# Performance work log

Measured on AMD Instinct MI355X. Metric: run time of the kernel, lower is better.

## Reference

```python
import jax, jax.numpy as jnp
import numpy as np
import math

N_HEADS = 16
D_HEAD = 64
D_MODEL = 1024
ROPE_THETA = 10000.0


def setup_inputs() -> dict:
    key = jax.random.key(0)
    k1, k2, k3 = jax.random.split(key, 3)
    B, T = 2, 2048
    x = jax.random.normal(k1, (B, T, D_MODEL), dtype=jnp.float32)
    # torch Linear(in, out) weight has shape (out, in); store transposed (in, out)
    # so forward is x @ w. Scale like default init to keep activations sane.
    w_qkv = jax.random.normal(k2, (D_MODEL, 3 * D_MODEL), dtype=jnp.float32) / math.sqrt(D_MODEL)
    w_o = jax.random.normal(k3, (D_MODEL, D_MODEL), dtype=jnp.float32) / math.sqrt(D_MODEL)
    return {"x": x, "w_qkv": w_qkv, "w_o": w_o}


def _build_rope(T, dtype):
    inv_freq = 1.0 / (ROPE_THETA ** (jnp.arange(0, D_HEAD, 2, dtype=jnp.float32) / D_HEAD))
    t = jnp.arange(T, dtype=jnp.float32)
    freqs = jnp.outer(t, inv_freq)            # [T, D_HEAD/2]
    emb = jnp.concatenate([freqs, freqs], -1)  # [T, D_HEAD]
    return jnp.cos(emb).astype(dtype), jnp.sin(emb).astype(dtype)


def _apply_rope(x, cos, sin):
    # x: [B, T, H, D_HEAD]; cos/sin broadcast as [1, T, 1, D_HEAD]
    x1, x2 = jnp.split(x, 2, axis=-1)
    rotated = jnp.concatenate([-x2, x1], axis=-1)
    return x * cos + rotated * sin


def reference(x, w_qkv, w_o):
    B, T, D = x.shape
    qkv = (x @ w_qkv).reshape(B, T, 3, N_HEADS, D_HEAD)
    q, k, v = qkv[:, :, 0], qkv[:, :, 1], qkv[:, :, 2]  # [B, T, H, Dh]
    cos, sin = _build_rope(T, x.dtype)
    cos = cos[None, :, None, :]
    sin = sin[None, :, None, :]
    q = _apply_rope(q, cos, sin)
    k = _apply_rope(k, cos, sin)
    scale = 1.0 / math.sqrt(D_HEAD)
    # full [B, H, T, T] scores (faithful to the manual matmul-softmax-matmul)
    attn = jnp.einsum("bthd,bshd->bhts", q, k) * scale
    attn = jax.nn.softmax(attn, axis=-1)
    out = jnp.einsum("bhts,bshd->bthd", attn, v).reshape(B, T, D)
    return out @ w_o
```

## Files before the change

kernel.cpp:

```cpp
#include <hip/hip_runtime.h>
#include <cstdint>

typedef unsigned short ushort_t;
typedef __attribute__((ext_vector_type(8))) short v8s;
typedef __attribute__((ext_vector_type(4))) short v4s;
typedef __attribute__((ext_vector_type(2))) unsigned v2u;
typedef __attribute__((ext_vector_type(4))) float v4f;

#define MFMA(a, b, c) __builtin_amdgcn_mfma_f32_16x16x32_bf16(a, b, c, 0, 0, 0)
#define QSCALE 0.18033688011112042f

__device__ __forceinline__ float bf2f(ushort_t u) {
    union { unsigned u; float f; } x; x.u = ((unsigned)u) << 16; return x.f;
}
__device__ __forceinline__ short f2bf(float f) {
    union { float f; unsigned u; } x; x.f = f;
    unsigned r = x.u + 0x7fffu + ((x.u >> 16) & 1u);
    return (short)(r >> 16);
}

__global__ void detect_dtype(const unsigned* __restrict__ x, int* __restrict__ flag) {
    __shared__ int cnt;
    if (threadIdx.x == 0) cnt = 0;
    __syncthreads();
    unsigned w = x[threadIdx.x];
    int e = (w >> 7) & 0xFF;
    int hit = ((e >= 96 && e <= 135) || (w & 0xFFFFu) == 0) ? 1 : 0;
    atomicAdd(&cnt, hit);
    __syncthreads();
    if (threadIdx.x == 0) *flag = (cnt >= 160) ? 1 : 0;
}

__global__ __launch_bounds__(256) void cvt_x(const void* __restrict__ xin,
                                             ushort_t* __restrict__ xb,
                                             const int* __restrict__ flagp, int n8) {
    int i = blockIdx.x * 256 + threadIdx.x;
    if (i >= n8) return;
    if (*flagp) {
        ((v8s*)xb)[i] = ((const v8s*)xin)[i];
    } else {
        const float* xf = (const float*)xin + (size_t)i * 8;
        v8s o;
        #pragma unroll
        for (int j = 0; j < 8; ++j) o[j] = f2bf(xf[j]);
        ((v8s*)xb)[i] = o;
    }
}

__global__ __launch_bounds__(256) void cvt_transpose(const void* __restrict__ in,
                                                     ushort_t* __restrict__ out,
                                                     const int* __restrict__ flagp,
                                                     int R, int C) {
    __shared__ ushort_t tile[32][33];
    int bx = blockIdx.x * 32, by = blockIdx.y * 32;
    int tx = threadIdx.x, ty = threadIdx.y;
    int isbf = *flagp;
    for (int i = ty; i < 32; i += 8) {
        size_t idx = (size_t)(by + i) * C + bx + tx;
        tile[i][tx] = isbf ? ((const ushort_t*)in)[idx]
                           : (ushort_t)f2bf(((const float*)in)[idx]);
    }
    __syncthreads();
    for (int i = ty; i < 32; i += 8) out[(size_t)(bx + i) * R + by + tx] = tile[tx][i];
}

__global__ __launch_bounds__(256) void rope_table(float* __restrict__ tab) {
    int idx = blockIdx.x * 256 + threadIdx.x;
    int t = idx >> 5, d = idx & 31;
    float inv_freq = __expf(-(float)d * 0.28782313662425575f);
    float ang = (float)t * inv_freq;
    float sn, cs;
    sincosf(ang, &sn, &cs);
    tab[t * 64 + d]      = bf2f((ushort_t)f2bf(cs));
    tab[t * 64 + 32 + d] = bf2f((ushort_t)f2bf(sn));
}

template <int MODE>
__global__ __launch_bounds__(256) void gemm_bt(const ushort_t* __restrict__ A,
                                               const ushort_t* __restrict__ BT,
                                               void* __restrict__ C,
                                               const int* __restrict__ flagp,
                                               int M, int N, int K,
                                               ushort_t* __restrict__ Qp,
                                               ushort_t* __restrict__ Kp,
                                               ushort_t* __restrict__ Vp,
                                               const float* __restrict__ tab) {
    __shared__ __align__(16) ushort_t As[128 * 32];
    __shared__ __align__(16) ushort_t Bs[128 * 32];
    int tid = threadIdx.x;
    int lane = tid & 63;
    int lr = lane & 15, lc = lane >> 4;
    int w = tid >> 6;
    int wr = (w >> 1) * 64, wc = (w & 1) * 64;
    int m0 = blockIdx.y * 128, n0 = blockIdx.x * 128;

    int c0 = tid, c1 = tid + 256;
    int r0 = c0 >> 2, s0 = c0 & 3;
    int r1 = c1 >> 2, s1 = c1 & 3;

    v4f acc[4][4] = {};

    for (int kt = 0; kt < K; kt += 32) {
        v8s a0 = *(const v8s*)(A + (size_t)(m0 + r0) * K + kt + s0 * 8);
        v8s a1 = *(const v8s*)(A + (size_t)(m0 + r1) * K + kt + s1 * 8);
        v8s b0 = *(const v8s*)(BT + (size_t)(n0 + r0) * K + kt + s0 * 8);
        v8s b1 = *(const v8s*)(BT + (size_t)(n0 + r1) * K + kt + s1 * 8);
        __syncthreads();
        *(v8s*)(As + (size_t)c0 * 8) = a0;
        *(v8s*)(As + (size_t)c1 * 8) = a1;
        *(v8s*)(Bs + (size_t)c0 * 8) = b0;
        *(v8s*)(Bs + (size_t)c1 * 8) = b1;
        __syncthreads();

        v8s af[4], bfr[4];
        #pragma unroll
        for (int i = 0; i < 4; ++i)
            af[i] = *(const v8s*)(As + (wr + i * 16 + lr) * 32 + lc * 8);
        #pragma unroll
        for (int j = 0; j < 4; ++j)
            bfr[j] = *(const v8s*)(Bs + (wc + j * 16 + lr) * 32 + lc * 8);
        #pragma unroll
        for (int i = 0; i < 4; ++i)
            #pragma unroll
            for (int j = 0; j < 4; ++j)
                acc[i][j] = MFMA(af[i], bfr[j], acc[i][j]);
    }

    if (MODE == 1) {
        int store_f32 = (*flagp == 0);
        #pragma unroll
        for (int i = 0; i < 4; ++i)
            #pragma unroll
            for (int j = 0; j < 4; ++j)
                #pragma unroll
                for (int r = 0; r < 4; ++r) {
                    int row = m0 + wr + i * 16 + lc * 4 + r;
                    int col = n0 + wc + j * 16 + lr;
                    if (store_f32)
                        ((float*)C)[(size_t)row * N + col] = acc[i][j][r];
                    else
                        ((ushort_t*)C)[(size_t)row * N + col] = (ushort_t)f2bf(acc[i][j][r]);
                }
    } else {
        int region = n0 >> 10;
        int h = ((n0 & 1023) + wc) >> 6;
        if (region < 2) {
            const float sc = (region == 0) ? QSCALE : 1.0f;
            ushort_t* dst = (region == 0) ? Qp : Kp;
            #pragma unroll
            for (int i = 0; i < 4; ++i)
                #pragma unroll
                for (int j = 0; j < 2; ++j) {
                    int d = j * 16 + lr;
                    #pragma unroll
                    for (int r = 0; r < 4; ++r) {
                        int tg = m0 + wr + i * 16 + lc * 4 + r;
                        int b = tg >> 11, tt = tg & 2047;
                        float cs = tab[tt * 64 + d], sn = tab[tt * 64 + 32 + d];
                        float x1 = acc[i][j][r], x2 = acc[i][j + 2][r];
                        size_t base = ((size_t)(b * 16 + h) * 2048 + tt) * 64 + d;
                        dst[base]      = (ushort_t)f2bf((x1 * cs - x2 * sn) * sc);
                        dst[base + 32] = (ushort_t)f2bf((x2 * cs + x1 * sn) * sc);
                    }
                }
        } else {
            #pragma unroll
            for (int i = 0; i < 4; ++i)
                #pragma unroll
                for (int j = 0; j < 4; ++j) {
                    int d = j * 16 + lr;
                    int tg0 = m0 + wr + i * 16 + lc * 4;
                    int b = tg0 >> 11, tt = tg0 & 2047;
                    v4s pk;
                    #pragma unroll
                    for (int r = 0; r < 4; ++r) pk[r] = f2bf(acc[i][j][r]);
                    size_t base = (size_t)(b * 16 + h) * 131072 + (size_t)(tt >> 5) * 2048
                                + (size_t)d * 32 + (tt & 31);
                    *(v4s*)(Vp + base) = pk;
                }
        }
    }
}

__global__ __launch_bounds__(256) void attn(const ushort_t* __restrict__ Qr,
                                            const ushort_t* __restrict__ Kr,
                                            const ushort_t* __restrict__ Vt,
                                            ushort_t* __restrict__ AO) {
    __shared__ __align__(16) char lds[53248];
    int tid = threadIdx.x, lane = tid & 63, W = tid >> 6;
    int lr = lane & 15, lc = lane >> 4;
    int qsub = W & 1, sh = W >> 1;
    int L = blockIdx.x;
    int bh = (L & 7) * 4 + ((L >> 3) & 3);
    int qt = L >> 5;
    int q0 = qt * 128 + qsub * 64;
    int b = bh >> 4, h = bh & 15;
    const ushort_t* Qb = Qr + ((size_t)bh * 2048 + q0) * 64;
    const ushort_t* Kb = Kr + (size_t)bh * 131072 + (size_t)sh * 65536;
    const ushort_t* Vb = Vt + (size_t)bh * 131072 + (size_t)sh * 65536;
    ushort_t* Pw  = (ushort_t*)(lds + 32768 + W * 5120);
    ushort_t* KsG = (ushort_t*)(lds + sh * 16384);
    ushort_t* VsG = (ushort_t*)(lds + sh * 16384 + 8192);

    int gt = tid & 127;
    int c0 = gt, c1 = gt + 128;
    int kr0 = c0 >> 3, kc0 = c0 & 7, kr1 = c1 >> 3, kc1 = c1 & 7;
    const ushort_t* Kg0 = Kb + (size_t)kr0 * 64 + kc0 * 8;
    const ushort_t* Kg1 = Kb + (size_t)kr1 * 64 + kc1 * 8;
    int kl0 = kr0 * 64 + (kc0 ^ (kr0 & 7)) * 8;
    int kl1 = kr1 * 64 + (kc1 ^ (kr1 & 7)) * 8;
    const ushort_t* Vg0 = Vb + (size_t)c0 * 8;
    const ushort_t* Vg1 = Vb + (size_t)c1 * 8;
    int vl0 = c0 * 8, vl1 = c1 * 8;

    v8s qf[4][2];
    #pragma unroll
    for (int jq = 0; jq < 4; ++jq)
        #pragma unroll
        for (int kk = 0; kk < 2; ++kk)
            qf[jq][kk] = *(const v8s*)(Qb + (size_t)(jq * 16 + lr) * 64 + kk * 32 + lc * 8);

    v4f o[4][4] = {};
    float li[4] = {0.f, 0.f, 0.f, 0.f};

    v8s ka = *(const v8s*)(Kg0), kb2 = *(const v8s*)(Kg1);
    v8s va = *(const v8s*)(Vg0), vb2 = *(const v8s*)(Vg1);
    *(v8s*)(KsG + kl0) = ka;
    *(v8s*)(KsG + kl1) = kb2;
    *(v8s*)(VsG + vl0) = va;
    *(v8s*)(VsG + vl1) = vb2;
    ka  = *(const v8s*)(Kg0 + 2048);
    kb2 = *(const v8s*)(Kg1 + 2048);
    va  = *(const v8s*)(Vg0 + 2048);
    vb2 = *(const v8s*)(Vg1 + 2048);
    __syncthreads();

    #pragma unroll 1
    for (int t = 0; t < 32; ++t) {
        int p = t & 1;
        const ushort_t* Kl = KsG + p * 2048;
        const ushort_t* Vl = VsG + p * 2048;

        v8s kf[2][2], vf[4];
        #pragma unroll
        for (int hh = 0; hh < 2; ++hh)
            #pragma unroll
            for (int kk = 0; kk < 2; ++kk)
                kf[hh][kk] = *(const v8s*)(Kl + (hh * 16 + lr) * 64 + (((kk * 4 + lc) ^ (lr & 7)) * 8));
        #pragma unroll
        for (int i = 0; i < 4; ++i)
            vf[i] = *(const v8s*)(Vl + (i * 16 + lr) * 32 + lc * 8);

        v4f St[2][4] = {};
        #pragma unroll
        for (int hh = 0; hh < 2; ++hh)
            #pragma unroll
            for (int jq = 0; jq < 4; ++jq) {
                St[hh][jq] = MFMA(kf[hh][0], qf[jq][0], St[hh][jq]);
                St[hh][jq] = MFMA(kf[hh][1], qf[jq][1], St[hh][jq]);
            }

        if (t + 1 < 32) {
            ushort_t* Kn = KsG + (p ^ 1) * 2048;
            ushort_t* Vn = VsG + (p ^ 1) * 2048;
            *(v8s*)(Kn + kl0) = ka;
            *(v8s*)(Kn + kl1) = kb2;
            *(v8s*)(Vn + vl0) = va;
            *(v8s*)(Vn + vl1) = vb2;
        }
        if (t + 2 < 32) {
            ka  = *(const v8s*)(Kg0 + (size_t)(t + 2) * 2048);
            kb2 = *(const v8s*)(Kg1 + (size_t)(t + 2) * 2048);
            va  = *(const v8s*)(Vg0 + (size_t)(t + 2) * 2048);
            vb2 = *(const v8s*)(Vg1 + (size_t)(t + 2) * 2048);
        }

        #pragma unroll
        for (int jq = 0; jq < 4; ++jq)
            #pragma unroll
            for (int hh = 0; hh < 2; ++hh) {
                #pragma unroll
                for (int r = 0; r < 4; ++r) {
                    float ev = __builtin_amdgcn_exp2f(St[hh][jq][r]);
                    St[hh][jq][r] = ev;
                    li[jq] += ev;
                }
                unsigned d0 = __builtin_amdgcn_perm(__float_as_uint(St[hh][jq][1]),
                                                    __float_as_uint(St[hh][jq][0]), 0x07060302u);
                unsigned d1 = __builtin_amdgcn_perm(__float_as_uint(St[hh][jq][3]),
                                                    __float_as_uint(St[hh][jq][2]), 0x07060302u);
                v2u pk = {d0, d1};
                *(v2u*)(Pw + (jq * 16 + lr) * 40 + hh * 16 + lc * 4) = pk;
            }
        __builtin_amdgcn_s_waitcnt(0xc07f);
        #pragma unroll
        for (int jq = 0; jq < 4; ++jq) {
            v8s pf = *(const v8s*)(Pw + (jq * 16 + lr) * 40 + lc * 8);
            #pragma unroll
            for (int i = 0; i < 4; ++i)
                o[i][jq] = MFMA(vf[i], pf, o[i][jq]);
        }
        __syncthreads();
    }

    #pragma unroll
    for (int jq = 0; jq < 4; ++jq) {
        li[jq] += __shfl_xor(li[jq], 16);
        li[jq] += __shfl_xor(li[jq], 32);
    }
    float* MO = (float*)(lds + qsub * 17408);
    float* Ml = (float*)(lds + 34816 + qsub * 256);
    __syncthreads();
    if (sh == 1) {
        #pragma unroll
        for (int jq = 0; jq < 4; ++jq) {
            #pragma unroll
            for (int i = 0; i < 4; ++i)
                *(v4f*)(MO + (jq * 16 + lr) * 68 + i * 16 + lc * 4) = o[i][jq];
            if (lc == 0) Ml[jq * 16 + lr] = li[jq];
        }
    }
    __syncthreads();
    if (sh == 0) {
        #pragma unroll
        for (int jq = 0; jq < 4; ++jq) {
            float inv = 1.0f / (li[jq] + Ml[jq * 16 + lr]);
            int t = q0 + jq * 16 + lr;
            #pragma unroll
            for (int i = 0; i < 4; ++i) {
                v4f m = *(const v4f*)(MO + (jq * 16 + lr) * 68 + i * 16 + lc * 4);
                v4s pk;
                #pragma unroll
                for (int r = 0; r < 4; ++r) pk[r] = f2bf((o[i][jq][r] + m[r]) * inv);
                *(v4s*)(AO + (size_t)(b * 2048 + t) * 1024 + h * 64 + i * 16 + lc * 4) = pk;
            }
        }
    }
}

extern "C" void kernel_launch(void* const* d_in, const int* in_sizes, int n_in,
                              void* d_out, int out_size, void* d_ws, size_t ws_size,
                              hipStream_t stream) {
    char* ws = (char*)d_ws;
    int*      flag  = (int*)ws;
    ushort_t* wqkvT = (ushort_t*)(ws + 256);
    ushort_t* woT   = (ushort_t*)(ws + 6291712);
    ushort_t* xb    = (ushort_t*)(ws + 8388864);
    ushort_t* Qr    = (ushort_t*)(ws + 16777472);
    ushort_t* Kr    = (ushort_t*)(ws + 25166080);
    ushort_t* Vt    = (ushort_t*)(ws + 33554688);
    ushort_t* AO    = (ushort_t*)(ws + 41943296);
    float*    tab   = (float*)(ws + 50331904);

    detect_dtype<<<1, 256, 0, stream>>>((const unsigned*)d_in[0], flag);
    rope_table<<<256, 256, 0, stream>>>(tab);
    cvt_x<<<2048, 256, 0, stream>>>(d_in[0], xb, flag, 524288);
    dim3 tb(32, 8);
    cvt_transpose<<<dim3(96, 32), tb, 0, stream>>>(d_in[1], wqkvT, flag, 1024, 3072);
    cvt_transpose<<<dim3(32, 32), tb, 0, stream>>>(d_in[2], woT, flag, 1024, 1024);
    gemm_bt<2><<<dim3(24, 32), 256, 0, stream>>>(xb, wqkvT, nullptr, flag, 4096, 3072, 1024,
                                                 Qr, Kr, Vt, tab);
    attn<<<512, 256, 0, stream>>>(Qr, Kr, Vt, AO);
    gemm_bt<1><<<dim3(8, 32), 256, 0, stream>>>(AO, woT, d_out, flag, 4096, 1024, 1024,
                                                nullptr, nullptr, nullptr, nullptr);
}
```

Measured before the change: 209.9 us.

## Use direct global-to-LDS loads in GEMM, swizzle blocks, raise MFMA priority

The GEMM tile loads now use global_load_lds to copy straight from global memory into shared memory, skipping the round trip through registers. Thread blocks are remapped with an XCD-style swizzle so neighbouring tiles land on the same chiplet for better L2 reuse. The attention kernel also wraps its MFMA sections in s_setprio to favour matrix issue. The swizzle assumes the grid size divides by 8, and the LDS layout must match the per-wave ordering of global_load_lds.

```diff
diff --git a/kernel.cpp b/kernel.cpp
--- a/kernel.cpp
+++ b/kernel.cpp
@@ -9,6 +9,10 @@
 
 #define MFMA(a, b, c) __builtin_amdgcn_mfma_f32_16x16x32_bf16(a, b, c, 0, 0, 0)
 #define QSCALE 0.18033688011112042f
+
+#define GLL(gp, lp) __builtin_amdgcn_global_load_lds(                        \
+    (const __attribute__((address_space(1))) void*)(gp),                     \
+    (__attribute__((address_space(3))) void*)(lp), 16, 0, 0)
 
 __device__ __forceinline__ float bf2f(ushort_t u) {
     union { unsigned u; float f; } x; x.u = ((unsigned)u) << 16; return x.f;
@@ -92,24 +96,34 @@
     int lr = lane & 15, lc = lane >> 4;
     int w = tid >> 6;
     int wr = (w >> 1) * 64, wc = (w & 1) * 64;
-    int m0 = blockIdx.y * 128, n0 = blockIdx.x * 128;
+
+    int nx = gridDim.x;
+    int orig = blockIdx.y * nx + blockIdx.x;
+    int cpx = (nx * gridDim.y) >> 3;
+    int swz = (orig & 7) * cpx + (orig >> 3);
+    int m0 = (swz / nx) * 128, n0 = (swz % nx) * 128;
 
     int c0 = tid, c1 = tid + 256;
     int r0 = c0 >> 2, s0 = c0 & 3;
     int r1 = c1 >> 2, s1 = c1 & 3;
 
+    const ushort_t* Ag0 = A + (size_t)(m0 + r0) * K + s0 * 8;
+    const ushort_t* Ag1 = A + (size_t)(m0 + r1) * K + s1 * 8;
+    const ushort_t* Bg0 = BT + (size_t)(n0 + r0) * K + s0 * 8;
+    const ushort_t* Bg1 = BT + (size_t)(n0 + r1) * K + s1 * 8;
+    ushort_t* Al0 = As + (size_t)(w * 64) * 8;
+    ushort_t* Al1 = As + (size_t)(256 + w * 64) * 8;
+    ushort_t* Bl0 = Bs + (size_t)(w * 64) * 8;
+    ushort_t* Bl1 = Bs + (size_t)(256 + w * 64) * 8;
+
     v4f acc[4][4] = {};
 
     for (int kt = 0; kt < K; kt += 32) {
-        v8s a0 = *(const v8s*)(A + (size_t)(m0 + r0) * K + kt + s0 * 8);
-        v8s a1 = *(const v8s*)(A + (size_t)(m0 + r1) * K + kt + s1 * 8);
-        v8s b0 = *(const v8s*)(BT + (size_t)(n0 + r0) * K + kt + s0 * 8);
-        v8s b1 = *(const v8s*)(BT + (size_t)(n0 + r1) * K + kt + s1 * 8);
         __syncthreads();
-        *(v8s*)(As + (size_t)c0 * 8) = a0;
-        *(v8s*)(As + (size_t)c1 * 8) = a1;
-        *(v8s*)(Bs + (size_t)c0 * 8) = b0;
-        *(v8s*)(Bs + (size_t)c1 * 8) = b1;
+        GLL(Ag0 + kt, Al0);
+        GLL(Ag1 + kt, Al1);
+        GLL(Bg0 + kt, Bl0);
+        GLL(Bg1 + kt, Bl1);
         __syncthreads();
 
         v8s af[4], bfr[4];
@@ -252,6 +266,7 @@
             vf[i] = *(const v8s*)(Vl + (i * 16 + lr) * 32 + lc * 8);
 
         v4f St[2][4] = {};
+        __builtin_amdgcn_s_setprio(1);
         #pragma unroll
         for (int hh = 0; hh < 2; ++hh)
             #pragma unroll
@@ -259,6 +274,7 @@
                 St[hh][jq] = MFMA(kf[hh][0], qf[jq][0], St[hh][jq]);
                 St[hh][jq] = MFMA(kf[hh][1], qf[jq][1], St[hh][jq]);
             }
+        __builtin_amdgcn_s_setprio(0);
 
         if (t + 1 < 32) {
             ushort_t* Kn = KsG + (p ^ 1) * 2048;
@@ -293,6 +309,7 @@
                 *(v2u*)(Pw + (jq * 16 + lr) * 40 + hh * 16 + lc * 4) = pk;
             }
         __builtin_amdgcn_s_waitcnt(0xc07f);
+        __builtin_amdgcn_s_setprio(1);
         #pragma unroll
         for (int jq = 0; jq < 4; ++jq) {
             v8s pf = *(const v8s*)(Pw + (jq * 16 + lr) * 40 + lc * 8);
@@ -300,6 +317,7 @@
             for (int i = 0; i < 4; ++i)
                 o[i][jq] = MFMA(vf[i], pf, o[i][jq]);
         }
+        __builtin_amdgcn_s_setprio(0);
         __syncthreads();
     }
 
```

Measured after the change: 209.3 us. About the same (-0.3%).
